# Kernel optimization log

Hardware: AMD Instinct MI355X
Metric: run time of the kernel (lower is better)

## Reference

```python
import jax, jax.numpy as jnp
import numpy as np

N_GRID = 262144   # grid vertices (all local, empty halo)
N_MESH = 40962    # icosahedral mesh level-6 vertices
N_EDGES = 524288  # mesh2grid bipartite edges
H = 128           # cfg.model.hidden_dim
LN_EPS = 1e-5


def layer_norm(x, g, b):
    m = jnp.mean(x, axis=-1, keepdims=True)
    v = jnp.var(x, axis=-1, keepdims=True)
    return (x - m) * jax.lax.rsqrt(v + LN_EPS) * g + b


def setup_inputs() -> dict:
    key = jax.random.key(0)
    ks = jax.random.split(key, 12)
    def w(k, shape, fan_in):
        return jax.random.normal(k, shape, jnp.float32) * (fan_in ** -0.5)
    return {
        "mesh2grid_edge_features": jax.random.normal(ks[0], (N_EDGES, H), jnp.float32),
        "grid_node_features": jax.random.normal(ks[1], (N_GRID, H), jnp.float32),
        "mesh_node_features": jax.random.normal(ks[2], (N_MESH, H), jnp.float32),
        # edge MLP: Linear(3H->H) -> SiLU -> Linear(H->H) -> LayerNorm, residual
        "edge_W1": w(ks[3], (3 * H, H), 3 * H), "edge_b1": jnp.zeros((H,), jnp.float32),
        "edge_W2": w(ks[4], (H, H), H), "edge_b2": jnp.zeros((H,), jnp.float32),
        "edge_ln_g": jnp.ones((H,), jnp.float32), "edge_ln_b": jnp.zeros((H,), jnp.float32),
        # node MLP: Linear(2H->H) -> SiLU -> Linear(H->H) -> LayerNorm
        "node_W1": w(ks[5], (2 * H, H), 2 * H), "node_b1": jnp.zeros((H,), jnp.float32),
        "node_W2": w(ks[6], (H, H), H), "node_b2": jnp.zeros((H,), jnp.float32),
        "node_ln_g": jnp.ones((H,), jnp.float32), "node_ln_b": jnp.zeros((H,), jnp.float32),
        "src_indices": jax.random.randint(ks[7], (N_EDGES,), 0, N_MESH, jnp.int32),
        "dst_indices": jax.random.randint(ks[8], (N_EDGES,), 0, N_GRID, jnp.int32),
    }


def reference(mesh2grid_edge_features, grid_node_features, mesh_node_features,
              edge_W1, edge_b1, edge_W2, edge_b2, edge_ln_g, edge_ln_b,
              node_W1, node_b1, node_W2, node_b2, node_ln_g, node_ln_b,
              src_indices, dst_indices):
    # --- edge block: gather src (mesh) / dst (grid), MLP, LN, residual ---
    src = mesh_node_features[src_indices]        # [E, H]  (augmented mesh == mesh, empty halo)
    dst = grid_node_features[dst_indices]        # [E, H]
    xe = jnp.concatenate([src, dst, mesh2grid_edge_features], axis=-1)  # [E, 3H]
    he = (jax.nn.silu(xe @ edge_W1 + edge_b1)) @ edge_W2 + edge_b2
    e_feats = mesh2grid_edge_features + layer_norm(he, edge_ln_g, edge_ln_b)  # [E, H]
    # --- node block: scatter-sum edges to grid nodes, MLP, LN ---
    agg = jax.ops.segment_sum(e_feats, dst_indices, num_segments=N_GRID)  # [N_grid, H]
    xn = jnp.concatenate([grid_node_features, agg], axis=-1)              # [N_grid, 2H]
    hn = (jax.nn.silu(xn @ node_W1 + node_b1)) @ node_W2 + node_b2
    n_feats = layer_norm(hn, node_ln_g, node_ln_b)
    return grid_node_features + n_feats
```

## Files before the change

### kernel.cpp

```cpp
#include <hip/hip_runtime.h>
#include <stdint.h>

#define HDIM 128
#define NGRID 262144
#define NMESH 40962
#define NEDGE 524288

typedef __attribute__((ext_vector_type(8))) short short8;
typedef __attribute__((ext_vector_type(4))) float f32x4;

__device__ __forceinline__ unsigned short f2bf(float f) {
  union { float f; uint32_t u; } v; v.f = f;
  uint32_t u = v.u;
  u += 0x7fffu + ((u >> 16) & 1u);
  return (unsigned short)(u >> 16);
}
__device__ __forceinline__ float bf2f(unsigned short h) {
  union { uint32_t u; float f; } v; v.u = ((uint32_t)h) << 16;
  return v.f;
}
__device__ __forceinline__ short8 cvt8(float4 a, float4 b) {
  short8 r;
  r[0] = (short)f2bf(a.x); r[1] = (short)f2bf(a.y);
  r[2] = (short)f2bf(a.z); r[3] = (short)f2bf(a.w);
  r[4] = (short)f2bf(b.x); r[5] = (short)f2bf(b.y);
  r[6] = (short)f2bf(b.z); r[7] = (short)f2bf(b.w);
  return r;
}

__global__ void pack_weights(const float* __restrict__ eW1, const float* __restrict__ eW2,
                             const float* __restrict__ nW1, const float* __restrict__ nW2,
                             unsigned short* __restrict__ ws)
{
  int i = blockIdx.x * 256 + threadIdx.x;
  unsigned short* eW1T = ws;
  unsigned short* eW2T = ws + 49152;
  unsigned short* nW1T = ws + 65536;
  unsigned short* nW2T = ws + 98304;
  if (i < 49152) {
    int c = i / 384, k = i % 384;
    eW1T[i] = f2bf(eW1[(size_t)k * 128 + c]);
  } else if (i < 65536) {
    int j = i - 49152; int c = j / 128, k = j % 128;
    eW2T[j] = f2bf(eW2[(size_t)k * 128 + c]);
  } else if (i < 98304) {
    int j = i - 65536; int c = j / 256, k = j % 256;
    nW1T[j] = f2bf(nW1[(size_t)k * 128 + c]);
  } else if (i < 114688) {
    int j = i - 98304; int c = j / 128, k = j % 128;
    nW2T[j] = f2bf(nW2[(size_t)k * 128 + c]);
  }
}

__global__ __launch_bounds__(256, 4)
void edge_kernel(const float* __restrict__ ef, const float* __restrict__ gridf,
                 const float* __restrict__ mesh,
                 const unsigned short* __restrict__ W1T, const unsigned short* __restrict__ W2T,
                 const float* __restrict__ b1, const float* __restrict__ b2,
                 const float* __restrict__ lng, const float* __restrict__ lnb,
                 const int* __restrict__ src, const int* __restrict__ dst,
                 float* __restrict__ agg)
{
  __shared__ __align__(16) unsigned short h1s[64][136];

  const int tid  = threadIdx.x;
  const int wave = tid >> 6;
  const int lane = tid & 63;
  const int l16  = lane & 15;
  const int g4   = lane >> 4;
  const int e0   = blockIdx.x * 64;
  const int arow = wave * 16 + l16;

  const int myS = src[e0 + arow];
  const int myD = dst[e0 + arow];
  const float* rowS = mesh  + (size_t)myS * HDIM;
  const float* rowD = gridf + (size_t)myD * HDIM;
  const float* rowE = ef    + (size_t)(e0 + arow) * HDIM;

  f32x4 acc[8];
  #pragma unroll
  for (int c = 0; c < 8; ++c) acc[c] = (f32x4){0.f, 0.f, 0.f, 0.f};

  const unsigned short* wl1 = W1T + (size_t)l16 * 384 + g4 * 8;

  #pragma unroll
  for (int part = 0; part < 3; ++part) {
    const float* base = (part == 0) ? rowS : (part == 1) ? rowD : rowE;
    #pragma unroll
    for (int kk = 0; kk < 4; ++kk) {
      const int ks = part * 4 + kk;
      const float* ap = base + kk * 32 + g4 * 8;
      float4 f0 = *reinterpret_cast<const float4*>(ap);
      float4 f1 = *reinterpret_cast<const float4*>(ap + 4);
      short8 a = cvt8(f0, f1);
      #pragma unroll
      for (int c = 0; c < 8; ++c) {
        short8 b = *reinterpret_cast<const short8*>(wl1 + (size_t)c * 16 * 384 + ks * 32);
        acc[c] = __builtin_amdgcn_mfma_f32_16x16x32_bf16(a, b, acc[c], 0, 0, 0);
      }
    }
  }

  #pragma unroll
  for (int c = 0; c < 8; ++c) {
    const int col = c * 16 + l16;
    float bb = b1[col];
    #pragma unroll
    for (int r = 0; r < 4; ++r) {
      float x = acc[c][r] + bb;
      float s = x / (1.f + __expf(-x));
      unsigned int h = f2bf(s);
      unsigned int other = __shfl_xor((int)h, 1);
      unsigned int packed = (l16 & 1) ? ((h << 16) | other) : ((other << 16) | h);
      if ((l16 & 1) == (r & 1)) {
        *reinterpret_cast<unsigned int*>(&h1s[wave * 16 + g4 * 4 + r][c * 16 + (l16 & ~1)]) = packed;
      }
    }
  }
  __syncthreads();

  f32x4 acc2[8];
  #pragma unroll
  for (int c = 0; c < 8; ++c) acc2[c] = (f32x4){0.f, 0.f, 0.f, 0.f};

  const unsigned short* wl2 = W2T + (size_t)l16 * 128 + g4 * 8;
  #pragma unroll
  for (int ks = 0; ks < 4; ++ks) {
    short8 a = *reinterpret_cast<const short8*>(&h1s[arow][ks * 32 + g4 * 8]);
    #pragma unroll
    for (int c = 0; c < 8; ++c) {
      short8 b = *reinterpret_cast<const short8*>(wl2 + (size_t)c * 16 * 128 + ks * 32);
      acc2[c] = __builtin_amdgcn_mfma_f32_16x16x32_bf16(a, b, acc2[c], 0, 0, 0);
    }
  }

  float vs[4] = {0.f, 0.f, 0.f, 0.f};
  float vq[4] = {0.f, 0.f, 0.f, 0.f};
  #pragma unroll
  for (int c = 0; c < 8; ++c) {
    float bb = b2[c * 16 + l16];
    #pragma unroll
    for (int r = 0; r < 4; ++r) {
      float x = acc2[c][r] + bb;
      acc2[c][r] = x;
      vs[r] += x;
      vq[r] += x * x;
    }
  }
  #pragma unroll
  for (int m = 1; m < 16; m <<= 1) {
    #pragma unroll
    for (int r = 0; r < 4; ++r) {
      vs[r] += __shfl_xor(vs[r], m);
      vq[r] += __shfl_xor(vq[r], m);
    }
  }
  float mean[4], rstd[4];
  #pragma unroll
  for (int r = 0; r < 4; ++r) {
    mean[r] = vs[r] * (1.f / 128.f);
    float var = vq[r] * (1.f / 128.f) - mean[r] * mean[r];
    rstd[r] = rsqrtf(var + 1e-5f);
  }
  int drow[4];
  #pragma unroll
  for (int r = 0; r < 4; ++r) drow[r] = dst[e0 + wave * 16 + g4 * 4 + r];

  #pragma unroll
  for (int c = 0; c < 8; ++c) {
    const int col = c * 16 + l16;
    float gg = lng[col], bb = lnb[col];
    #pragma unroll
    for (int r = 0; r < 4; ++r) {
      const int row = wave * 16 + g4 * 4 + r;
      float y = (acc2[c][r] - mean[r]) * rstd[r] * gg + bb;
      float e = ef[(size_t)(e0 + row) * HDIM + col] + y;
      unsafeAtomicAdd(&agg[(size_t)drow[r] * HDIM + col], e);
    }
  }
}

__global__ __launch_bounds__(256, 4)
void node_kernel(const float* __restrict__ gridf,
                 const unsigned short* __restrict__ W1T, const unsigned short* __restrict__ W2T,
                 const float* __restrict__ b1, const float* __restrict__ b2,
                 const float* __restrict__ lng, const float* __restrict__ lnb,
                 float* __restrict__ out)
{
  __shared__ __align__(16) unsigned short h1s[64][136];

  const int tid  = threadIdx.x;
  const int wave = tid >> 6;
  const int lane = tid & 63;
  const int l16  = lane & 15;
  const int g4   = lane >> 4;
  const int n0   = blockIdx.x * 64;
  const int arow = wave * 16 + l16;

  const float* rowG = gridf + (size_t)(n0 + arow) * HDIM;
  const float* rowA = out   + (size_t)(n0 + arow) * HDIM;

  f32x4 acc[8];
  #pragma unroll
  for (int c = 0; c < 8; ++c) acc[c] = (f32x4){0.f, 0.f, 0.f, 0.f};

  const unsigned short* wl1 = W1T + (size_t)l16 * 256 + g4 * 8;

  #pragma unroll
  for (int part = 0; part < 2; ++part) {
    const float* base = (part == 0) ? rowG : rowA;
    #pragma unroll
    for (int kk = 0; kk < 4; ++kk) {
      const int ks = part * 4 + kk;
      const float* ap = base + kk * 32 + g4 * 8;
      float4 f0 = *reinterpret_cast<const float4*>(ap);
      float4 f1 = *reinterpret_cast<const float4*>(ap + 4);
      short8 a = cvt8(f0, f1);
      #pragma unroll
      for (int c = 0; c < 8; ++c) {
        short8 b = *reinterpret_cast<const short8*>(wl1 + (size_t)c * 16 * 256 + ks * 32);
        acc[c] = __builtin_amdgcn_mfma_f32_16x16x32_bf16(a, b, acc[c], 0, 0, 0);
      }
    }
  }

  #pragma unroll
  for (int c = 0; c < 8; ++c) {
    const int col = c * 16 + l16;
    float bb = b1[col];
    #pragma unroll
    for (int r = 0; r < 4; ++r) {
      float x = acc[c][r] + bb;
      float s = x / (1.f + __expf(-x));
      unsigned int h = f2bf(s);
      unsigned int other = __shfl_xor((int)h, 1);
      unsigned int packed = (l16 & 1) ? ((h << 16) | other) : ((other << 16) | h);
      if ((l16 & 1) == (r & 1)) {
        *reinterpret_cast<unsigned int*>(&h1s[wave * 16 + g4 * 4 + r][c * 16 + (l16 & ~1)]) = packed;
      }
    }
  }
  __syncthreads();

  f32x4 acc2[8];
  #pragma unroll
  for (int c = 0; c < 8; ++c) acc2[c] = (f32x4){0.f, 0.f, 0.f, 0.f};

  const unsigned short* wl2 = W2T + (size_t)l16 * 128 + g4 * 8;
  #pragma unroll
  for (int ks = 0; ks < 4; ++ks) {
    short8 a = *reinterpret_cast<const short8*>(&h1s[arow][ks * 32 + g4 * 8]);
    #pragma unroll
    for (int c = 0; c < 8; ++c) {
      short8 b = *reinterpret_cast<const short8*>(wl2 + (size_t)c * 16 * 128 + ks * 32);
      acc2[c] = __builtin_amdgcn_mfma_f32_16x16x32_bf16(a, b, acc2[c], 0, 0, 0);
    }
  }

  float vs[4] = {0.f, 0.f, 0.f, 0.f};
  float vq[4] = {0.f, 0.f, 0.f, 0.f};
  #pragma unroll
  for (int c = 0; c < 8; ++c) {
    float bb = b2[c * 16 + l16];
    #pragma unroll
    for (int r = 0; r < 4; ++r) {
      float x = acc2[c][r] + bb;
      acc2[c][r] = x;
      vs[r] += x;
      vq[r] += x * x;
    }
  }
  #pragma unroll
  for (int m = 1; m < 16; m <<= 1) {
    #pragma unroll
    for (int r = 0; r < 4; ++r) {
      vs[r] += __shfl_xor(vs[r], m);
      vq[r] += __shfl_xor(vq[r], m);
    }
  }
  float mean[4], rstd[4];
  #pragma unroll
  for (int r = 0; r < 4; ++r) {
    mean[r] = vs[r] * (1.f / 128.f);
    float var = vq[r] * (1.f / 128.f) - mean[r] * mean[r];
    rstd[r] = rsqrtf(var + 1e-5f);
  }
  #pragma unroll
  for (int c = 0; c < 8; ++c) {
    const int col = c * 16 + l16;
    float gg = lng[col], bb = lnb[col];
    #pragma unroll
    for (int r = 0; r < 4; ++r) {
      const int row = wave * 16 + g4 * 4 + r;
      size_t idx = (size_t)(n0 + row) * HDIM + col;
      float y = (acc2[c][r] - mean[r]) * rstd[r] * gg + bb;
      out[idx] = gridf[idx] + y;
    }
  }
}

extern "C" void kernel_launch(void* const* d_in, const int* in_sizes, int n_in,
                              void* d_out, int out_size, void* d_ws, size_t ws_size,
                              hipStream_t stream)
{
  (void)in_sizes; (void)n_in; (void)out_size; (void)ws_size;
  const float* ef   = (const float*)d_in[0];
  const float* grid = (const float*)d_in[1];
  const float* mesh = (const float*)d_in[2];
  const float* eW1  = (const float*)d_in[3];
  const float* eb1  = (const float*)d_in[4];
  const float* eW2  = (const float*)d_in[5];
  const float* eb2  = (const float*)d_in[6];
  const float* elng = (const float*)d_in[7];
  const float* elnb = (const float*)d_in[8];
  const float* nW1  = (const float*)d_in[9];
  const float* nb1  = (const float*)d_in[10];
  const float* nW2  = (const float*)d_in[11];
  const float* nb2  = (const float*)d_in[12];
  const float* nlng = (const float*)d_in[13];
  const float* nlnb = (const float*)d_in[14];
  const int* src    = (const int*)d_in[15];
  const int* dst    = (const int*)d_in[16];
  float* out = (float*)d_out;
  unsigned short* ws = (unsigned short*)d_ws;

  hipMemsetAsync(out, 0, (size_t)NGRID * HDIM * sizeof(float), stream);
  pack_weights<<<448, 256, 0, stream>>>(eW1, eW2, nW1, nW2, ws);
  edge_kernel<<<NEDGE / 64, 256, 0, stream>>>(ef, grid, mesh,
      ws, ws + 49152, eb1, eb2, elng, elnb, src, dst, out);
  node_kernel<<<NGRID / 64, 256, 0, stream>>>(grid,
      ws + 65536, ws + 98304, nb1, nb2, nlng, nlnb, out);
}
```

Measured before the change: 957.4 us.

## Rewrite edge/node kernels with LDS-resident swizzled weights, 32x32 MFMA, bf16 atomic aggregation

Both kernels are rewritten. The packed weights are copied once per block into 128KB of swizzled LDS. Each wave computes the transposed product with 32x32x16 bf16 MFMA, keeping the hidden activations in registers through cross-half shuffles instead of a shared-memory round trip. When the workspace is large enough, scatter-sum aggregation switches to packed bf16 atomics into a half-size buffer, which cuts atomic traffic but lowers the precision of the accumulation. Larger 512-thread blocks and vectorized float4 epilogues are also used.

```diff
diff --git a/kernel.cpp b/kernel.cpp
--- a/kernel.cpp
+++ b/kernel.cpp
@@ -3,298 +3,348 @@
 
 #define HDIM 128
 #define NGRID 262144
-#define NMESH 40962
 #define NEDGE 524288
 
 typedef __attribute__((ext_vector_type(8))) short short8;
-typedef __attribute__((ext_vector_type(4))) float f32x4;
-
-__device__ __forceinline__ unsigned short f2bf(float f) {
+typedef __attribute__((ext_vector_type(16))) float f32x16;
+
+static __device__ __forceinline__ unsigned int f2bf_u(float f) {
   union { float f; uint32_t u; } v; v.f = f;
   uint32_t u = v.u;
   u += 0x7fffu + ((u >> 16) & 1u);
-  return (unsigned short)(u >> 16);
-}
-__device__ __forceinline__ float bf2f(unsigned short h) {
-  union { uint32_t u; float f; } v; v.u = ((uint32_t)h) << 16;
-  return v.f;
-}
-__device__ __forceinline__ short8 cvt8(float4 a, float4 b) {
+  return u >> 16;
+}
+static __device__ __forceinline__ unsigned short f2bf(float f) { return (unsigned short)f2bf_u(f); }
+static __device__ __forceinline__ unsigned int pack2bf(float a, float b) {
+  return f2bf_u(a) | (f2bf_u(b) << 16);
+}
+static __device__ __forceinline__ short8 cvt8(const float* p) {
+  float4 f0 = *(const float4*)p;
+  float4 f1 = *(const float4*)(p + 4);
   short8 r;
-  r[0] = (short)f2bf(a.x); r[1] = (short)f2bf(a.y);
-  r[2] = (short)f2bf(a.z); r[3] = (short)f2bf(a.w);
-  r[4] = (short)f2bf(b.x); r[5] = (short)f2bf(b.y);
-  r[6] = (short)f2bf(b.z); r[7] = (short)f2bf(b.w);
+  r[0] = (short)f2bf_u(f0.x); r[1] = (short)f2bf_u(f0.y);
+  r[2] = (short)f2bf_u(f0.z); r[3] = (short)f2bf_u(f0.w);
+  r[4] = (short)f2bf_u(f1.x); r[5] = (short)f2bf_u(f1.y);
+  r[6] = (short)f2bf_u(f1.z); r[7] = (short)f2bf_u(f1.w);
   return r;
 }
+static __device__ __forceinline__ void atom_pk_bf16(unsigned short* p, unsigned int v) {
+  asm volatile("global_atomic_pk_add_bf16 %0, %1, off" :: "v"(p), "v"(v) : "memory");
+}
+
+union U8 { unsigned int u[4]; short8 s; };
 
 __global__ void pack_weights(const float* __restrict__ eW1, const float* __restrict__ eW2,
                              const float* __restrict__ nW1, const float* __restrict__ nW2,
-                             unsigned short* __restrict__ ws)
+                             unsigned char* __restrict__ wbase)
 {
   int i = blockIdx.x * 256 + threadIdx.x;
-  unsigned short* eW1T = ws;
-  unsigned short* eW2T = ws + 49152;
-  unsigned short* nW1T = ws + 65536;
-  unsigned short* nW2T = ws + 98304;
   if (i < 49152) {
-    int c = i / 384, k = i % 384;
-    eW1T[i] = f2bf(eW1[(size_t)k * 128 + c]);
+    int row = i / 384, k = i % 384;
+    int db = row * 768 + ((2 * k) ^ ((row & 7) << 4));
+    *(unsigned short*)(wbase + db) = f2bf(eW1[(size_t)k * 128 + row]);
   } else if (i < 65536) {
-    int j = i - 49152; int c = j / 128, k = j % 128;
-    eW2T[j] = f2bf(eW2[(size_t)k * 128 + c]);
+    int j = i - 49152; int row = j / 128, k = j % 128;
+    int db = row * 256 + ((2 * k) ^ ((row & 7) << 4));
+    *(unsigned short*)(wbase + 98304 + db) = f2bf(eW2[(size_t)k * 128 + row]);
   } else if (i < 98304) {
-    int j = i - 65536; int c = j / 256, k = j % 256;
-    nW1T[j] = f2bf(nW1[(size_t)k * 128 + c]);
+    int j = i - 65536; int row = j / 256, k = j % 256;
+    int db = row * 512 + ((2 * k) ^ ((row & 7) << 4));
+    *(unsigned short*)(wbase + 131072 + db) = f2bf(nW1[(size_t)k * 128 + row]);
   } else if (i < 114688) {
-    int j = i - 98304; int c = j / 128, k = j % 128;
-    nW2T[j] = f2bf(nW2[(size_t)k * 128 + c]);
-  }
-}
-
-__global__ __launch_bounds__(256, 4)
+    int j = i - 98304; int row = j / 128, k = j % 128;
+    int db = row * 256 + ((2 * k) ^ ((row & 7) << 4));
+    *(unsigned short*)(wbase + 196608 + db) = f2bf(nW2[(size_t)k * 128 + row]);
+  }
+}
+
+template<bool BF16AGG>
+__global__ __launch_bounds__(512, 2)
 void edge_kernel(const float* __restrict__ ef, const float* __restrict__ gridf,
                  const float* __restrict__ mesh,
-                 const unsigned short* __restrict__ W1T, const unsigned short* __restrict__ W2T,
+                 const unsigned char* __restrict__ wbase,
                  const float* __restrict__ b1, const float* __restrict__ b2,
                  const float* __restrict__ lng, const float* __restrict__ lnb,
                  const int* __restrict__ src, const int* __restrict__ dst,
-                 float* __restrict__ agg)
+                 unsigned short* __restrict__ aggb, float* __restrict__ aggf)
 {
-  __shared__ __align__(16) unsigned short h1s[64][136];
-
-  const int tid  = threadIdx.x;
-  const int wave = tid >> 6;
-  const int lane = tid & 63;
-  const int l16  = lane & 15;
-  const int g4   = lane >> 4;
-  const int e0   = blockIdx.x * 64;
-  const int arow = wave * 16 + l16;
-
-  const int myS = src[e0 + arow];
-  const int myD = dst[e0 + arow];
-  const float* rowS = mesh  + (size_t)myS * HDIM;
-  const float* rowD = gridf + (size_t)myD * HDIM;
-  const float* rowE = ef    + (size_t)(e0 + arow) * HDIM;
-
-  f32x4 acc[8];
-  #pragma unroll
-  for (int c = 0; c < 8; ++c) acc[c] = (f32x4){0.f, 0.f, 0.f, 0.f};
-
-  const unsigned short* wl1 = W1T + (size_t)l16 * 384 + g4 * 8;
-
-  #pragma unroll
-  for (int part = 0; part < 3; ++part) {
-    const float* base = (part == 0) ? rowS : (part == 1) ? rowD : rowE;
-    #pragma unroll
-    for (int kk = 0; kk < 4; ++kk) {
-      const int ks = part * 4 + kk;
-      const float* ap = base + kk * 32 + g4 * 8;
-      float4 f0 = *reinterpret_cast<const float4*>(ap);
-      float4 f1 = *reinterpret_cast<const float4*>(ap + 4);
-      short8 a = cvt8(f0, f1);
-      #pragma unroll
-      for (int c = 0; c < 8; ++c) {
-        short8 b = *reinterpret_cast<const short8*>(wl1 + (size_t)c * 16 * 384 + ks * 32);
-        acc[c] = __builtin_amdgcn_mfma_f32_16x16x32_bf16(a, b, acc[c], 0, 0, 0);
-      }
-    }
-  }
-
-  #pragma unroll
-  for (int c = 0; c < 8; ++c) {
-    const int col = c * 16 + l16;
-    float bb = b1[col];
-    #pragma unroll
-    for (int r = 0; r < 4; ++r) {
-      float x = acc[c][r] + bb;
-      float s = x / (1.f + __expf(-x));
-      unsigned int h = f2bf(s);
-      unsigned int other = __shfl_xor((int)h, 1);
-      unsigned int packed = (l16 & 1) ? ((h << 16) | other) : ((other << 16) | h);
-      if ((l16 & 1) == (r & 1)) {
-        *reinterpret_cast<unsigned int*>(&h1s[wave * 16 + g4 * 4 + r][c * 16 + (l16 & ~1)]) = packed;
-      }
-    }
+  __shared__ __align__(16) unsigned char smem[131072];
+
+  const int tid = threadIdx.x;
+  {
+    const uint4* gsrc = (const uint4*)wbase;
+    uint4* ldst = (uint4*)smem;
+    #pragma unroll
+    for (int i = 0; i < 16; ++i) ldst[tid + i * 512] = gsrc[tid + i * 512];
   }
   __syncthreads();
 
-  f32x4 acc2[8];
-  #pragma unroll
-  for (int c = 0; c < 8; ++c) acc2[c] = (f32x4){0.f, 0.f, 0.f, 0.f};
-
-  const unsigned short* wl2 = W2T + (size_t)l16 * 128 + g4 * 8;
-  #pragma unroll
-  for (int ks = 0; ks < 4; ++ks) {
-    short8 a = *reinterpret_cast<const short8*>(&h1s[arow][ks * 32 + g4 * 8]);
-    #pragma unroll
-    for (int c = 0; c < 8; ++c) {
-      short8 b = *reinterpret_cast<const short8*>(wl2 + (size_t)c * 16 * 128 + ks * 32);
-      acc2[c] = __builtin_amdgcn_mfma_f32_16x16x32_bf16(a, b, acc2[c], 0, 0, 0);
-    }
-  }
-
-  float vs[4] = {0.f, 0.f, 0.f, 0.f};
-  float vq[4] = {0.f, 0.f, 0.f, 0.f};
-  #pragma unroll
-  for (int c = 0; c < 8; ++c) {
-    float bb = b2[c * 16 + l16];
-    #pragma unroll
-    for (int r = 0; r < 4; ++r) {
-      float x = acc2[c][r] + bb;
-      acc2[c][r] = x;
-      vs[r] += x;
-      vq[r] += x * x;
-    }
-  }
-  #pragma unroll
-  for (int m = 1; m < 16; m <<= 1) {
-    #pragma unroll
-    for (int r = 0; r < 4; ++r) {
-      vs[r] += __shfl_xor(vs[r], m);
-      vq[r] += __shfl_xor(vq[r], m);
-    }
-  }
-  float mean[4], rstd[4];
-  #pragma unroll
-  for (int r = 0; r < 4; ++r) {
-    mean[r] = vs[r] * (1.f / 128.f);
-    float var = vq[r] * (1.f / 128.f) - mean[r] * mean[r];
-    rstd[r] = rsqrtf(var + 1e-5f);
-  }
-  int drow[4];
-  #pragma unroll
-  for (int r = 0; r < 4; ++r) drow[r] = dst[e0 + wave * 16 + g4 * 4 + r];
-
-  #pragma unroll
-  for (int c = 0; c < 8; ++c) {
-    const int col = c * 16 + l16;
-    float gg = lng[col], bb = lnb[col];
-    #pragma unroll
-    for (int r = 0; r < 4; ++r) {
-      const int row = wave * 16 + g4 * 4 + r;
-      float y = (acc2[c][r] - mean[r]) * rstd[r] * gg + bb;
-      float e = ef[(size_t)(e0 + row) * HDIM + col] + y;
-      unsafeAtomicAdd(&agg[(size_t)drow[r] * HDIM + col], e);
-    }
-  }
-}
-
-__global__ __launch_bounds__(256, 4)
+  const int wv = tid >> 6, ln = tid & 63, l31 = ln & 31, hi = ln >> 5;
+  const int job = blockIdx.x * 8 + wv;
+  const int swz = (l31 & 7) << 4;
+
+  const float* rowS[2]; const float* rowD[2]; const float* rowE[2]; int dI[2];
+  #pragma unroll
+  for (int t = 0; t < 2; ++t) {
+    int e = job * 64 + t * 32 + l31;
+    int s = src[e]; int d = dst[e]; dI[t] = d;
+    rowS[t] = mesh  + (size_t)s * HDIM;
+    rowD[t] = gridf + (size_t)d * HDIM;
+    rowE[t] = ef    + (size_t)e * HDIM;
+  }
+
+  f32x16 acc1[8];
+  #pragma unroll
+  for (int i = 0; i < 8; ++i) acc1[i] = (f32x16)(0.f);
+
+  #pragma unroll
+  for (int ks = 0; ks < 24; ++ks) {
+    short8 A[4];
+    #pragma unroll
+    for (int c = 0; c < 4; ++c) {
+      int addr = (32 * c + l31) * 768 + ((32 * ks + 16 * hi) ^ swz);
+      A[c] = *(const short8*)(smem + addr);
+    }
+    short8 Bt[2];
+    #pragma unroll
+    for (int t = 0; t < 2; ++t) {
+      const float* base = (ks < 8) ? rowS[t] : (ks < 16) ? rowD[t] : rowE[t];
+      Bt[t] = cvt8(base + (ks & 7) * 16 + hi * 8);
+    }
+    #pragma unroll
+    for (int t = 0; t < 2; ++t)
+      #pragma unroll
+      for (int c = 0; c < 4; ++c)
+        acc1[t * 4 + c] = __builtin_amdgcn_mfma_f32_32x32x16_bf16(A[c], Bt[t], acc1[t * 4 + c], 0, 0, 0);
+  }
+
+  #pragma unroll
+  for (int t = 0; t < 2; ++t) {
+    #pragma unroll
+    for (int c = 0; c < 4; ++c) {
+      #pragma unroll
+      for (int q = 0; q < 4; ++q) {
+        float4 b1q = *(const float4*)(b1 + 32 * c + 8 * q + 4 * hi);
+        #pragma unroll
+        for (int i = 0; i < 4; ++i) {
+          float x = acc1[t * 4 + c][q * 4 + i] + b1q[i];
+          acc1[t * 4 + c][q * 4 + i] = x / (1.f + __expf(-x));
+        }
+      }
+    }
+    U8 B2[8];
+    #pragma unroll
+    for (int w = 0; w < 8; ++w) {
+      int c = w >> 1, h = w & 1;
+      const f32x16& a = acc1[t * 4 + c];
+      unsigned P1a = pack2bf(a[8 * h + 0], a[8 * h + 1]);
+      unsigned P1b = pack2bf(a[8 * h + 2], a[8 * h + 3]);
+      unsigned P2a = pack2bf(a[8 * h + 4], a[8 * h + 5]);
+      unsigned P2b = pack2bf(a[8 * h + 6], a[8 * h + 7]);
+      unsigned sA = hi ? P1a : P2a, sB = hi ? P1b : P2b;
+      unsigned rA = (unsigned)__shfl_xor((int)sA, 32);
+      unsigned rB = (unsigned)__shfl_xor((int)sB, 32);
+      B2[w].u[0] = hi ? rA : P1a;
+      B2[w].u[1] = hi ? rB : P1b;
+      B2[w].u[2] = hi ? P2a : rA;
+      B2[w].u[3] = hi ? P2b : rB;
+    }
+    f32x16 acc2[4];
+    #pragma unroll
+    for (int i = 0; i < 4; ++i) acc2[i] = (f32x16)(0.f);
+    #pragma unroll
+    for (int c2 = 0; c2 < 4; ++c2) {
+      #pragma unroll
+      for (int w = 0; w < 8; ++w) {
+        int addr = 98304 + (32 * c2 + l31) * 256 + ((32 * w + 16 * hi) ^ swz);
+        short8 A2 = *(const short8*)(smem + addr);
+        acc2[c2] = __builtin_amdgcn_mfma_f32_32x32x16_bf16(A2, B2[w].s, acc2[c2], 0, 0, 0);
+      }
+    }
+    float vs = 0.f, vq = 0.f;
+    #pragma unroll
+    for (int c2 = 0; c2 < 4; ++c2) {
+      #pragma unroll
+      for (int q = 0; q < 4; ++q) {
+        float4 b2q = *(const float4*)(b2 + 32 * c2 + 8 * q + 4 * hi);
+        #pragma unroll
+        for (int i = 0; i < 4; ++i) {
+          float x = acc2[c2][q * 4 + i] + b2q[i];
+          acc2[c2][q * 4 + i] = x;
+          vs += x; vq += x * x;
+        }
+      }
+    }
+    vs += __shfl_xor(vs, 32);
+    vq += __shfl_xor(vq, 32);
+    float mean = vs * (1.f / 128.f);
+    float rstd = rsqrtf(vq * (1.f / 128.f) - mean * mean + 1e-5f);
+
+    #pragma unroll
+    for (int c2 = 0; c2 < 4; ++c2) {
+      #pragma unroll
+      for (int q = 0; q < 4; ++q) {
+        int colb = 32 * c2 + 8 * q + 4 * hi;
+        float4 g4 = *(const float4*)(lng + colb);
+        float4 bb4 = *(const float4*)(lnb + colb);
+        float4 e4 = *(const float4*)(rowE[t] + colb);
+        float e0 = e4.x + (acc2[c2][q * 4 + 0] - mean) * rstd * g4.x + bb4.x;
+        float e1 = e4.y + (acc2[c2][q * 4 + 1] - mean) * rstd * g4.y + bb4.y;
+        float e2 = e4.z + (acc2[c2][q * 4 + 2] - mean) * rstd * g4.z + bb4.z;
+        float e3 = e4.w + (acc2[c2][q * 4 + 3] - mean) * rstd * g4.w + bb4.w;
+        if (BF16AGG) {
+          unsigned short* p = aggb + (size_t)dI[t] * HDIM + colb;
+          atom_pk_bf16(p, pack2bf(e0, e1));
+          atom_pk_bf16(p + 2, pack2bf(e2, e3));
+        } else {
+          float* p = aggf + (size_t)dI[t] * HDIM + colb;
+          unsafeAtomicAdd(p + 0, e0);
+          unsafeAtomicAdd(p + 1, e1);
+          unsafeAtomicAdd(p + 2, e2);
+          unsafeAtomicAdd(p + 3, e3);
+        }
+      }
+    }
+  }
+}
+
+template<bool BF16AGG>
+__global__ __launch_bounds__(512, 2)
 void node_kernel(const float* __restrict__ gridf,
-                 const unsigned short* __restrict__ W1T, const unsigned short* __restrict__ W2T,
+                 const unsigned char* __restrict__ wbase,
                  const float* __restrict__ b1, const float* __restrict__ b2,
                  const float* __restrict__ lng, const float* __restrict__ lnb,
+                 const unsigned short* __restrict__ aggb, const float* __restrict__ aggf,
                  float* __restrict__ out)
 {
-  __shared__ __align__(16) unsigned short h1s[64][136];
-
-  const int tid  = threadIdx.x;
-  const int wave = tid >> 6;
-  const int lane = tid & 63;
-  const int l16  = lane & 15;
-  const int g4   = lane >> 4;
-  const int n0   = blockIdx.x * 64;
-  const int arow = wave * 16 + l16;
-
-  const float* rowG = gridf + (size_t)(n0 + arow) * HDIM;
-  const float* rowA = out   + (size_t)(n0 + arow) * HDIM;
-
-  f32x4 acc[8];
-  #pragma unroll
-  for (int c = 0; c < 8; ++c) acc[c] = (f32x4){0.f, 0.f, 0.f, 0.f};
-
-  const unsigned short* wl1 = W1T + (size_t)l16 * 256 + g4 * 8;
-
-  #pragma unroll
-  for (int part = 0; part < 2; ++part) {
-    const float* base = (part == 0) ? rowG : rowA;
-    #pragma unroll
-    for (int kk = 0; kk < 4; ++kk) {
-      const int ks = part * 4 + kk;
-      const float* ap = base + kk * 32 + g4 * 8;
-      float4 f0 = *reinterpret_cast<const float4*>(ap);
-      float4 f1 = *reinterpret_cast<const float4*>(ap + 4);
-      short8 a = cvt8(f0, f1);
-      #pragma unroll
-      for (int c = 0; c < 8; ++c) {
-        short8 b = *reinterpret_cast<const short8*>(wl1 + (size_t)c * 16 * 256 + ks * 32);
-        acc[c] = __builtin_amdgcn_mfma_f32_16x16x32_bf16(a, b, acc[c], 0, 0, 0);
-      }
-    }
-  }
-
-  #pragma unroll
-  for (int c = 0; c < 8; ++c) {
-    const int col = c * 16 + l16;
-    float bb = b1[col];
-    #pragma unroll
-    for (int r = 0; r < 4; ++r) {
-      float x = acc[c][r] + bb;
-      float s = x / (1.f + __expf(-x));
-      unsigned int h = f2bf(s);
-      unsigned int other = __shfl_xor((int)h, 1);
-      unsigned int packed = (l16 & 1) ? ((h << 16) | other) : ((other << 16) | h);
-      if ((l16 & 1) == (r & 1)) {
-        *reinterpret_cast<unsigned int*>(&h1s[wave * 16 + g4 * 4 + r][c * 16 + (l16 & ~1)]) = packed;
-      }
-    }
+  __shared__ __align__(16) unsigned char smem[98304];
+
+  const int tid = threadIdx.x;
+  {
+    const uint4* gsrc = (const uint4*)wbase;
+    uint4* ldst = (uint4*)smem;
+    #pragma unroll
+    for (int i = 0; i < 12; ++i) ldst[tid + i * 512] = gsrc[tid + i * 512];
   }
   __syncthreads();
 
-  f32x4 acc2[8];
-  #pragma unroll
-  for (int c = 0; c < 8; ++c) acc2[c] = (f32x4){0.f, 0.f, 0.f, 0.f};
-
-  const unsigned short* wl2 = W2T + (size_t)l16 * 128 + g4 * 8;
-  #pragma unroll
-  for (int ks = 0; ks < 4; ++ks) {
-    short8 a = *reinterpret_cast<const short8*>(&h1s[arow][ks * 32 + g4 * 8]);
-    #pragma unroll
-    for (int c = 0; c < 8; ++c) {
-      short8 b = *reinterpret_cast<const short8*>(wl2 + (size_t)c * 16 * 128 + ks * 32);
-      acc2[c] = __builtin_amdgcn_mfma_f32_16x16x32_bf16(a, b, acc2[c], 0, 0, 0);
-    }
-  }
-
-  float vs[4] = {0.f, 0.f, 0.f, 0.f};
-  float vq[4] = {0.f, 0.f, 0.f, 0.f};
-  #pragma unroll
-  for (int c = 0; c < 8; ++c) {
-    float bb = b2[c * 16 + l16];
-    #pragma unroll
-    for (int r = 0; r < 4; ++r) {
-      float x = acc2[c][r] + bb;
-      acc2[c][r] = x;
-      vs[r] += x;
-      vq[r] += x * x;
-    }
-  }
-  #pragma unroll
-  for (int m = 1; m < 16; m <<= 1) {
-    #pragma unroll
-    for (int r = 0; r < 4; ++r) {
-      vs[r] += __shfl_xor(vs[r], m);
-      vq[r] += __shfl_xor(vq[r], m);
-    }
-  }
-  float mean[4], rstd[4];
-  #pragma unroll
-  for (int r = 0; r < 4; ++r) {
-    mean[r] = vs[r] * (1.f / 128.f);
-    float var = vq[r] * (1.f / 128.f) - mean[r] * mean[r];
-    rstd[r] = rsqrtf(var + 1e-5f);
-  }
-  #pragma unroll
-  for (int c = 0; c < 8; ++c) {
-    const int col = c * 16 + l16;
-    float gg = lng[col], bb = lnb[col];
-    #pragma unroll
-    for (int r = 0; r < 4; ++r) {
-      const int row = wave * 16 + g4 * 4 + r;
-      size_t idx = (size_t)(n0 + row) * HDIM + col;
-      float y = (acc2[c][r] - mean[r]) * rstd[r] * gg + bb;
-      out[idx] = gridf[idx] + y;
+  const int wv = tid >> 6, ln = tid & 63, l31 = ln & 31, hi = ln >> 5;
+  const int job = blockIdx.x * 8 + wv;
+  const int swz = (l31 & 7) << 4;
+
+  int nIdx[2];
+  #pragma unroll
+  for (int t = 0; t < 2; ++t) nIdx[t] = job * 64 + t * 32 + l31;
+
+  f32x16 acc1[8];
+  #pragma unroll
+  for (int i = 0; i < 8; ++i) acc1[i] = (f32x16)(0.f);
+
+  #pragma unroll
+  for (int ks = 0; ks < 16; ++ks) {
+    short8 A[4];
+    #pragma unroll
+    for (int c = 0; c < 4; ++c) {
+      int addr = (32 * c + l31) * 512 + ((32 * ks + 16 * hi) ^ swz);
+      A[c] = *(const short8*)(smem + addr);
+    }
+    short8 Bt[2];
+    #pragma unroll
+    for (int t = 0; t < 2; ++t) {
+      if (ks < 8) {
+        Bt[t] = cvt8(gridf + (size_t)nIdx[t] * HDIM + ks * 16 + hi * 8);
+      } else {
+        if (BF16AGG) {
+          Bt[t] = *(const short8*)(aggb + (size_t)nIdx[t] * HDIM + (ks - 8) * 16 + hi * 8);
+        } else {
+          Bt[t] = cvt8(aggf + (size_t)nIdx[t] * HDIM + (ks - 8) * 16 + hi * 8);
+        }
+      }
+    }
+    #pragma unroll
+    for (int t = 0; t < 2; ++t)
+      #pragma unroll
+      for (int c = 0; c < 4; ++c)
+        acc1[t * 4 + c] = __builtin_amdgcn_mfma_f32_32x32x16_bf16(A[c], Bt[t], acc1[t * 4 + c], 0, 0, 0);
+  }
+
+  #pragma unroll
+  for (int t = 0; t < 2; ++t) {
+    #pragma unroll
+    for (int c = 0; c < 4; ++c) {
+      #pragma unroll
+      for (int q = 0; q < 4; ++q) {
+        float4 b1q = *(const float4*)(b1 + 32 * c + 8 * q + 4 * hi);
+        #pragma unroll
+        for (int i = 0; i < 4; ++i) {
+          float x = acc1[t * 4 + c][q * 4 + i] + b1q[i];
+          acc1[t * 4 + c][q * 4 + i] = x / (1.f + __expf(-x));
+        }
+      }
+    }
+    U8 B2[8];
+    #pragma unroll
+    for (int w = 0; w < 8; ++w) {
+      int c = w >> 1, h = w & 1;
+      const f32x16& a = acc1[t * 4 + c];
+      unsigned P1a = pack2bf(a[8 * h + 0], a[8 * h + 1]);
+      unsigned P1b = pack2bf(a[8 * h + 2], a[8 * h + 3]);
+      unsigned P2a = pack2bf(a[8 * h + 4], a[8 * h + 5]);
+      unsigned P2b = pack2bf(a[8 * h + 6], a[8 * h + 7]);
+      unsigned sA = hi ? P1a : P2a, sB = hi ? P1b : P2b;
+      unsigned rA = (unsigned)__shfl_xor((int)sA, 32);
+      unsigned rB = (unsigned)__shfl_xor((int)sB, 32);
+      B2[w].u[0] = hi ? rA : P1a;
+      B2[w].u[1] = hi ? rB : P1b;
+      B2[w].u[2] = hi ? P2a : rA;
+      B2[w].u[3] = hi ? P2b : rB;
+    }
+    f32x16 acc2[4];
+    #pragma unroll
+    for (int i = 0; i < 4; ++i) acc2[i] = (f32x16)(0.f);
+    #pragma unroll
+    for (int c2 = 0; c2 < 4; ++c2) {
+      #pragma unroll
+      for (int w = 0; w < 8; ++w) {
+        int addr = 65536 + (32 * c2 + l31) * 256 + ((32 * w + 16 * hi) ^ swz);
+        short8 A2 = *(const short8*)(smem + addr);
+        acc2[c2] = __builtin_amdgcn_mfma_f32_32x32x16_bf16(A2, B2[w].s, acc2[c2], 0, 0, 0);
+      }
+    }
+    float vs = 0.f, vq = 0.f;
+    #pragma unroll
+    for (int c2 = 0; c2 < 4; ++c2) {
+      #pragma unroll
+      for (int q = 0; q < 4; ++q) {
+        float4 b2q = *(const float4*)(b2 + 32 * c2 + 8 * q + 4 * hi);
+        #pragma unroll
+        for (int i = 0; i < 4; ++i) {
+          float x = acc2[c2][q * 4 + i] + b2q[i];
+          acc2[c2][q * 4 + i] = x;
+          vs += x; vq += x * x;
+        }
+      }
+    }
+    vs += __shfl_xor(vs, 32);
+    vq += __shfl_xor(vq, 32);
+    float mean = vs * (1.f / 128.f);
+    float rstd = rsqrtf(vq * (1.f / 128.f) - mean * mean + 1e-5f);
+
+    #pragma unroll
+    for (int c2 = 0; c2 < 4; ++c2) {
+      #pragma unroll
+      for (int q = 0; q < 4; ++q) {
+        int colb = 32 * c2 + 8 * q + 4 * hi;
+        float4 g4 = *(const float4*)(lng + colb);
+        float4 bb4 = *(const float4*)(lnb + colb);
+        float4 gr = *(const float4*)(gridf + (size_t)nIdx[t] * HDIM + colb);
+        float4 res;
+        res.x = gr.x + (acc2[c2][q * 4 + 0] - mean) * rstd * g4.x + bb4.x;
+        res.y = gr.y + (acc2[c2][q * 4 + 1] - mean) * rstd * g4.y + bb4.y;
+        res.z = gr.z + (acc2[c2][q * 4 + 2] - mean) * rstd * g4.z + bb4.z;
+        res.w = gr.w + (acc2[c2][q * 4 + 3] - mean) * rstd * g4.w + bb4.w;
+        *(float4*)(out + (size_t)nIdx[t] * HDIM + colb) = res;
+      }
     }
   }
 }
@@ -303,7 +353,7 @@
                               void* d_out, int out_size, void* d_ws, size_t ws_size,
                               hipStream_t stream)
 {
-  (void)in_sizes; (void)n_in; (void)out_size; (void)ws_size;
+  (void)in_sizes; (void)n_in; (void)out_size;
   const float* ef   = (const float*)d_in[0];
   const float* grid = (const float*)d_in[1];
   const float* mesh = (const float*)d_in[2];
@@ -322,12 +372,27 @@
   const int* src    = (const int*)d_in[15];
   const int* dst    = (const int*)d_in[16];
   float* out = (float*)d_out;
-  unsigned short* ws = (unsigned short*)d_ws;
-
-  hipMemsetAsync(out, 0, (size_t)NGRID * HDIM * sizeof(float), stream);
-  pack_weights<<<448, 256, 0, stream>>>(eW1, eW2, nW1, nW2, ws);
-  edge_kernel<<<NEDGE / 64, 256, 0, stream>>>(ef, grid, mesh,
-      ws, ws + 49152, eb1, eb2, elng, elnb, src, dst, out);
-  node_kernel<<<NGRID / 64, 256, 0, stream>>>(grid,
-      ws + 65536, ws + 98304, nb1, nb2, nlng, nlnb, out);
-}
+
+  const size_t AGG_BYTES = (size_t)NGRID * HDIM * 2;
+  const size_t W_BYTES   = 229376;
+  bool bf16agg = ws_size >= AGG_BYTES + W_BYTES;
+
+  unsigned char* wsb = (unsigned char*)d_ws;
+  unsigned short* aggb = (unsigned short*)wsb;
+  unsigned char* wbase = bf16agg ? (wsb + AGG_BYTES) : wsb;
+
+  pack_weights<<<448, 256, 0, stream>>>(eW1, eW2, nW1, nW2, wbase);
+  if (bf16agg) {
+    hipMemsetAsync(aggb, 0, AGG_BYTES, stream);
+    edge_kernel<true><<<1024, 512, 0, stream>>>(ef, grid, mesh, wbase,
+        eb1, eb2, elng, elnb, src, dst, aggb, nullptr);
+    node_kernel<true><<<512, 512, 0, stream>>>(grid, wbase + 131072,
+        nb1, nb2, nlng, nlnb, aggb, nullptr, out);
+  } else {
+    hipMemsetAsync(out, 0, (size_t)NGRID * HDIM * sizeof(float), stream);
+    edge_kernel<false><<<1024, 512, 0, stream>>>(ef, grid, mesh, wbase,
+        eb1, eb2, elng, elnb, src, dst, nullptr, out);
+    node_kernel<false><<<512, 512, 0, stream>>>(grid, wbase + 131072,
+        nb1, nb2, nlng, nlnb, nullptr, out, out);
+  }
+}
```

After: 1.175 ms. 1.23x slower.
